# Optimization experiments

Hardware: AMD Instinct MI355X
Metric: run time of the kernel (lower is better)

The kernel has to match this reference:

```python
import jax, jax.numpy as jnp
import numpy as np

B, NW = 1024, 300
N = NW // 3          # 100 tokens (keypoints)
E = 5                # token dim after cat of PE(2): 3 + 2
H, D, L = 4, 64, 3   # heads, d_attention, layers


def setup_inputs() -> dict:
    key = jax.random.key(0)
    ks = jax.random.split(key, 8)
    s = jnp.float32(0.1)
    x = jax.random.normal(ks[0], (B, NW), dtype=jnp.float32)
    Wq = jax.random.normal(ks[1], (L, H, D, E), dtype=jnp.float32) * s  # per-head W_Q (no bias)
    Wk = jax.random.normal(ks[2], (L, H, D, E), dtype=jnp.float32) * s
    Wv = jax.random.normal(ks[3], (L, H, D, E), dtype=jnp.float32) * s
    Wo = jax.random.normal(ks[4], (L, E, H * D), dtype=jnp.float32) * s  # MHA output proj (no bias)
    Wf = jax.random.normal(ks[5], (L, E, E), dtype=jnp.float32) * s      # FFN linear
    bf = jax.random.normal(ks[6], (L, E), dtype=jnp.float32) * s
    g1 = jnp.ones((L, E), dtype=jnp.float32)
    b1 = jnp.zeros((L, E), dtype=jnp.float32)
    g2 = jnp.ones((L, E), dtype=jnp.float32)
    b2 = jnp.zeros((L, E), dtype=jnp.float32)
    return dict(x=x, Wq=Wq, Wk=Wk, Wv=Wv, Wo=Wo, Wf=Wf, bf=bf,
                g1=g1, b1=b1, g2=g2, b2=b2)


def _layer_norm(x, g, b, eps=1e-5):
    mu = jnp.mean(x, axis=-1, keepdims=True)
    var = jnp.mean((x - mu) ** 2, axis=-1, keepdims=True)  # biased, like torch LN
    return (x - mu) / jnp.sqrt(var + eps) * g + b


def reference(x, Wq, Wk, Wv, Wo, Wf, bf, g1, b1, g2, b2):
    kp = x.reshape(B, N, 3)                      # 'b (n d) -> b n d', d=3
    mask = kp[:, :, -1] > 0                      # [B,N] keypoint confidence mask
    # PositionalEncoding(d_model=2, kind='cat'): div_term=[1] -> pe=[sin(pos),cos(pos)]
    pos = jnp.arange(N, dtype=jnp.float32)
    pe = jnp.stack([jnp.sin(pos), jnp.cos(pos)], axis=-1)         # [N,2]
    out = jnp.concatenate([kp, jnp.broadcast_to(pe, (B, N, 2))], axis=-1)  # [B,N,5]
    out = jnp.where(mask[:, :, None], out, jnp.float32(0.0))      # out[~mask]=0

    pair = mask[:, None, None, :] & mask[:, None, :, None]        # [B,1,N,N]
    neg = -jnp.finfo(jnp.float32).max
    scale = jnp.float32(1.0 / np.sqrt(D))
    for l in range(L):
        # per-head projections (heads vectorized over h)
        q = jnp.einsum('bne,hde->bhnd', out, Wq[l])
        k = jnp.einsum('bne,hde->bhnd', out, Wk[l])
        v = jnp.einsum('bne,hde->bhnd', out, Wv[l])
        dots = jnp.einsum('bhid,bhjd->bhij', q, k) * scale        # [B,H,N,N]
        dots = jnp.where(pair, dots, neg)
        attn = jax.nn.softmax(dots, axis=-1)
        o = jnp.einsum('bhij,bhjd->bhid', attn, v)                # [B,H,N,D]
        o = o.transpose(0, 2, 1, 3).reshape(B, N, H * D)          # concat heads
        attn_out = o @ Wo[l].T                                    # [B,N,E]
        ln1 = _layer_norm(attn_out + out, g1[l], b1[l])
        ffn = jax.nn.relu(ln1 @ Wf[l].T + bf[l])
        out = _layer_norm(ffn + ln1, g2[l], b2[l])
    return out
```

## Files before the change

### kernel.cpp

```cpp
#include <hip/hip_runtime.h>
#include <math.h>

#define NTOK 100
#define EDIM 5
#define NH   4
#define NL   3
#define DD   64
#define BLK  256

__global__ void precompute_mp(const float* __restrict__ Wq,
                              const float* __restrict__ Wk,
                              const float* __restrict__ Wv,
                              const float* __restrict__ Wo,
                              float* __restrict__ mp) {
  const int blk = blockIdx.x;
  const int which = blk / 12;
  const int rem = blk % 12;
  const int l = rem / 4, h = rem % 4;
  const int t = threadIdx.x;

  __shared__ float A[320];
  __shared__ float Bsh[320];

  const float* wa = (which ? Wv : Wq) + (l*NH + h)*DD*EDIM;
  for (int r = t; r < 320; r += 64) A[r] = wa[r];
  if (which == 0) {
    const float* wk = Wk + (l*NH + h)*DD*EDIM;
    for (int r = t; r < 320; r += 64) Bsh[r] = wk[r];
  } else {
    for (int r = t; r < 320; r += 64) {
      int f = r >> 6, d = r & 63;
      Bsh[r] = Wo[(l*EDIM + f)*(NH*DD) + h*DD + d];
    }
  }
  __syncthreads();
  if (t < 25) {
    int e = t / 5, f = t % 5;
    float acc = 0.f;
    if (which == 0) {
      #pragma unroll 8
      for (int d = 0; d < DD; ++d) acc += A[d*5+e] * Bsh[d*5+f];
      acc *= 0.125f;
    } else {
      #pragma unroll 8
      for (int d = 0; d < DD; ++d) acc += A[d*5+e] * Bsh[f*64+d];
    }
    mp[which*960 + ((l*NH + h)*EDIM + e)*8 + f] = acc;
  }
}

__global__ __launch_bounds__(BLK) void encoder_kernel(
    const float* __restrict__ x,
    const float* __restrict__ mp,
    const float* __restrict__ Wf,
    const float* __restrict__ bfv,
    const float* __restrict__ g1,
    const float* __restrict__ b1,
    const float* __restrict__ g2,
    const float* __restrict__ b2,
    float* __restrict__ out)
{
  const int b = blockIdx.x, t = threadIdx.x;

  __shared__ float4 s_MP4[480];
  __shared__ float4 s_o4[NTOK+2];
  __shared__ float  s_o1[NTOK+2];
  __shared__ float4 s_w4[2][NH][NTOK+2];
  __shared__ float2 s_w2[2][NH][NTOK+2];
  __shared__ int    s_cidx[NTOK];
  __shared__ unsigned long long s_bal[2];

  const float* mpf = (const float*)s_MP4;

  for (int r = t; r < 480; r += BLK) s_MP4[r] = ((const float4*)mp)[r];

  float k0=0.f, k1=0.f, k2=0.f, msk=0.f;
  if (t < NTOK) {
    k0 = x[b*300 + 3*t];
    k1 = x[b*300 + 3*t + 1];
    k2 = x[b*300 + 3*t + 2];
    msk = (k2 > 0.f) ? 1.f : 0.f;
  }
  unsigned long long bal = __ballot(t < NTOK && msk != 0.f);
  if (t == 0)  s_bal[0] = bal;
  if (t == 64) s_bal[1] = bal;
  __syncthreads();
  const unsigned long long bw0 = s_bal[0], bw1 = s_bal[1];
  const int nm = __popcll(bw0) + __popcll(bw1);
  if (t < NTOK) {
    int lane = t & 63;
    unsigned long long lm = (lane == 0) ? 0ull : ((1ull << lane) - 1ull);
    int pre = (t < 64) ? __popcll(bw0 & lm) : (__popcll(bw0) + __popcll(bw1 & lm));
    if (msk != 0.f) {
      s_o4[pre] = make_float4(k0, k1, k2, sinf((float)t));
      s_o1[pre] = cosf((float)t);
      s_cidx[t] = pre;
    } else {
      s_cidx[t] = nm;
    }
  }
  if (t == 0) {
    s_o4[nm]   = make_float4(0.f,0.f,0.f,0.f); s_o1[nm]   = 0.f;
    s_o4[nm+1] = make_float4(0.f,0.f,0.f,0.f); s_o1[nm+1] = 0.f;
  }
  __syncthreads();

  const int hp   = (nm + 2) >> 1;
  const int natt = NH * hp;
  const int nsplit = (2*natt <= BLK) ? 2 : 1;
  const bool task = (t < natt*nsplit);
  int h = 0, i0 = 0, i1 = 0, i1r = 0, jlo = 0, jhi = 0;
  bool rep0 = false, rep1 = false, w1ok = false;
  if (task) {
    int g  = t / natt;
    int tt = t - g*natt;
    h = tt / hp; i0 = tt - h*hp; i1 = i0 + hp;
    i1r = (i1 <= nm) ? i1 : nm;
    w1ok = (i1 <= nm);
    rep0 = (i0 == nm); rep1 = (i1 == nm);
    int jmid = nm >> 1;
    if (nsplit == 2) { jlo = g ? jmid : 0; jhi = g ? nm : jmid; }
    else             { jlo = 0; jhi = nm; }
  }
  const int wg = task ? (t / natt) : 0;

  for (int l = 0; l < NL; ++l) {
    if (task) {
      const float* Mh = mpf + ((l*NH + h)*EDIM)*8;
      float4 oA = s_o4[i0];  float oA4 = s_o1[i0];
      float4 oB = s_o4[i1r]; float oB4 = s_o1[i1r];
      float oa[5] = {oA.x, oA.y, oA.z, oA.w, oA4};
      float ob[5] = {oB.x, oB.y, oB.z, oB.w, oB4};
      float a0[5], a1[5];
      #pragma unroll
      for (int f = 0; f < 5; ++f) { a0[f] = 0.f; a1[f] = 0.f; }
      #pragma unroll
      for (int e = 0; e < 5; ++e) {
        float4 mr = *(const float4*)(Mh + e*8); float m4 = Mh[e*8+4];
        float va = oa[e], vb = ob[e];
        a0[0] += va*mr.x; a0[1] += va*mr.y; a0[2] += va*mr.z; a0[3] += va*mr.w; a0[4] += va*m4;
        a1[0] += vb*mr.x; a1[1] += vb*mr.y; a1[2] += vb*mr.z; a1[3] += vb*mr.w; a1[4] += vb*m4;
      }

      float ls0=0.f, ls1=0.f;
      float w00=0.f,w01=0.f,w02=0.f,w03=0.f,w04=0.f;
      float w10=0.f,w11=0.f,w12=0.f,w13=0.f,w14=0.f;
      #pragma unroll 4
      for (int j = jlo; j < jhi; ++j) {
        float4 oj = s_o4[j]; float oe = s_o1[j];
        float s0 = a0[0]*oj.x + a0[1]*oj.y + a0[2]*oj.z + a0[3]*oj.w + a0[4]*oe;
        float s1 = a1[0]*oj.x + a1[1]*oj.y + a1[2]*oj.z + a1[3]*oj.w + a1[4]*oe;
        float p0 = rep0 ? 1.f : __expf(s0);
        float p1 = rep1 ? 1.f : __expf(s1);
        ls0 += p0; ls1 += p1;
        w00 += p0*oj.x; w01 += p0*oj.y; w02 += p0*oj.z; w03 += p0*oj.w; w04 += p0*oe;
        w10 += p1*oj.x; w11 += p1*oj.y; w12 += p1*oj.z; w13 += p1*oj.w; w14 += p1*oe;
      }
      s_w4[wg][h][i0] = make_float4(w00, w01, w02, w03);
      s_w2[wg][h][i0] = make_float2(w04, ls0);
      if (w1ok) {
        s_w4[wg][h][i1] = make_float4(w10, w11, w12, w13);
        s_w2[wg][h][i1] = make_float2(w14, ls1);
      }
    }
    __syncthreads();

    if (t <= nm) {
      int i = t;
      bool rep = (i == nm);
      float4 ov = s_o4[i]; float ov4 = s_o1[i];
      float o[5] = {ov.x, ov.y, ov.z, ov.w, ov4};
      float wext = rep ? (float)(NTOK - nm) : 0.f;
      float c[5] = {0.f, 0.f, 0.f, 0.f, 0.f};
      #pragma unroll
      for (int hh = 0; hh < NH; ++hh) {
        float4 wa = s_w4[0][hh][i]; float2 wb = s_w2[0][hh][i];
        float w[5] = {wa.x, wa.y, wa.z, wa.w, wb.x};
        float ls = wb.y;
        if (nsplit == 2) {
          float4 wa2 = s_w4[1][hh][i]; float2 wb2 = s_w2[1][hh][i];
          w[0] += wa2.x; w[1] += wa2.y; w[2] += wa2.z; w[3] += wa2.w; w[4] += wb2.x;
          ls += wb2.y;
        }
        #pragma unroll
        for (int e = 0; e < 5; ++e) w[e] += wext * o[e];
        float inv = 1.f / (rep ? (float)NTOK : ls);
        const float* Ph = mpf + 960 + ((l*NH + hh)*EDIM)*8;
        #pragma unroll
        for (int e = 0; e < 5; ++e) {
          float4 pr = *(const float4*)(Ph + e*8); float p4 = Ph[e*8+4];
          float we = w[e] * inv;
          c[0] += we*pr.x; c[1] += we*pr.y; c[2] += we*pr.z; c[3] += we*pr.w; c[4] += we*p4;
        }
      }
      float y[5];
      #pragma unroll
      for (int e = 0; e < 5; ++e) y[e] = o[e] + c[e];
      float mu = 0.2f*(y[0]+y[1]+y[2]+y[3]+y[4]);
      float var = 0.f;
      #pragma unroll
      for (int e = 0; e < 5; ++e) { float d = y[e]-mu; var += d*d; }
      var *= 0.2f;
      float inv = 1.f / sqrtf(var + 1e-5f);
      float ln1[5];
      #pragma unroll
      for (int e = 0; e < 5; ++e) ln1[e] = (y[e]-mu)*inv*g1[l*5+e] + b1[l*5+e];
      float r2[5];
      #pragma unroll
      for (int e = 0; e < 5; ++e) {
        float acc = bfv[l*5+e];
        #pragma unroll
        for (int f = 0; f < 5; ++f) acc += ln1[f]*Wf[(l*5+e)*5+f];
        acc = acc > 0.f ? acc : 0.f;
        r2[e] = acc + ln1[e];
      }
      float mu2 = 0.2f*(r2[0]+r2[1]+r2[2]+r2[3]+r2[4]);
      float var2 = 0.f;
      #pragma unroll
      for (int e = 0; e < 5; ++e) { float d = r2[e]-mu2; var2 += d*d; }
      var2 *= 0.2f;
      float inv2 = 1.f / sqrtf(var2 + 1e-5f);
      float no0 = (r2[0]-mu2)*inv2*g2[l*5+0] + b2[l*5+0];
      float no1 = (r2[1]-mu2)*inv2*g2[l*5+1] + b2[l*5+1];
      float no2 = (r2[2]-mu2)*inv2*g2[l*5+2] + b2[l*5+2];
      float no3 = (r2[3]-mu2)*inv2*g2[l*5+3] + b2[l*5+3];
      float no4 = (r2[4]-mu2)*inv2*g2[l*5+4] + b2[l*5+4];
      s_o4[i] = make_float4(no0, no1, no2, no3);
      s_o1[i] = no4;
    }
    __syncthreads();
  }

  for (int r = t; r < NTOK*EDIM; r += BLK) {
    int i = r / EDIM;
    int e = r - i*EDIM;
    int c = s_cidx[i];
    float v = (e < 4) ? ((const float*)&s_o4[c])[e] : s_o1[c];
    out[b*(NTOK*EDIM) + r] = v;
  }
}

extern "C" void kernel_launch(void* const* d_in, const int* in_sizes, int n_in,
                              void* d_out, int out_size, void* d_ws, size_t ws_size,
                              hipStream_t stream) {
  const float* x  = (const float*)d_in[0];
  const float* Wq = (const float*)d_in[1];
  const float* Wk = (const float*)d_in[2];
  const float* Wv = (const float*)d_in[3];
  const float* Wo = (const float*)d_in[4];
  const float* Wf = (const float*)d_in[5];
  const float* bf = (const float*)d_in[6];
  const float* g1 = (const float*)d_in[7];
  const float* b1 = (const float*)d_in[8];
  const float* g2 = (const float*)d_in[9];
  const float* b2 = (const float*)d_in[10];
  float* outp = (float*)d_out;
  float* mp   = (float*)d_ws;

  precompute_mp<<<24, 64, 0, stream>>>(Wq, Wk, Wv, Wo, mp);
  encoder_kernel<<<1024, BLK, 0, stream>>>(x, mp, Wf, bf, g1, b1, g2, b2, outp);
}
```

Measured before the change: 119.2 us.

## Map one wavefront per batch element and drop block barriers

The encoder kernel now processes four batch elements per block, one per 64-lane wavefront. Each lane owns a masked token and loops over all keys for all four heads, with a second token-per-lane path when more than 63 tokens survive the mask. This removes the per-layer __syncthreads and the cross-thread partial-sum exchange through shared memory. Attention scores are pre-scaled by log2(e) so the kernel can call the hardware exp2 directly. The cost is a quarter as many waves, leaving less latency hiding, and more serial work per lane.

```diff
diff --git a/kernel.cpp b/kernel.cpp
--- a/kernel.cpp
+++ b/kernel.cpp
@@ -7,6 +7,7 @@
 #define NL   3
 #define DD   64
 #define BLK  256
+#define LOG2E 1.4426950408889634f
 
 __global__ void precompute_mp(const float* __restrict__ Wq,
                               const float* __restrict__ Wk,
@@ -49,7 +50,7 @@
   }
 }
 
-__global__ __launch_bounds__(BLK) void encoder_kernel(
+__global__ __launch_bounds__(BLK, 1) void encoder_kernel(
     const float* __restrict__ x,
     const float* __restrict__ mp,
     const float* __restrict__ Wf,
@@ -60,183 +61,216 @@
     const float* __restrict__ b2,
     float* __restrict__ out)
 {
-  const int b = blockIdx.x, t = threadIdx.x;
-
-  __shared__ float4 s_MP4[480];
-  __shared__ float4 s_o4[NTOK+2];
-  __shared__ float  s_o1[NTOK+2];
-  __shared__ float4 s_w4[2][NH][NTOK+2];
-  __shared__ float2 s_w2[2][NH][NTOK+2];
-  __shared__ int    s_cidx[NTOK];
-  __shared__ unsigned long long s_bal[2];
-
-  const float* mpf = (const float*)s_MP4;
-
-  for (int r = t; r < 480; r += BLK) s_MP4[r] = ((const float4*)mp)[r];
-
-  float k0=0.f, k1=0.f, k2=0.f, msk=0.f;
-  if (t < NTOK) {
-    k0 = x[b*300 + 3*t];
-    k1 = x[b*300 + 3*t + 1];
-    k2 = x[b*300 + 3*t + 2];
-    msk = (k2 > 0.f) ? 1.f : 0.f;
-  }
-  unsigned long long bal = __ballot(t < NTOK && msk != 0.f);
-  if (t == 0)  s_bal[0] = bal;
-  if (t == 64) s_bal[1] = bal;
+  const int wv   = threadIdx.x >> 6;
+  const int lane = threadIdx.x & 63;
+  const int b    = blockIdx.x * 4 + wv;
+
+  __shared__ float s_mp[1920];
+  __shared__ float s_st[4][NTOK+1][8];
+  __shared__ int   s_cidx[4][NTOK];
+
+  for (int r = threadIdx.x; r < 480; r += BLK)
+    ((float4*)s_mp)[r] = ((const float4*)mp)[r];
   __syncthreads();
-  const unsigned long long bw0 = s_bal[0], bw1 = s_bal[1];
-  const int nm = __popcll(bw0) + __popcll(bw1);
-  if (t < NTOK) {
-    int lane = t & 63;
-    unsigned long long lm = (lane == 0) ? 0ull : ((1ull << lane) - 1ull);
-    int pre = (t < 64) ? __popcll(bw0 & lm) : (__popcll(bw0) + __popcll(bw1 & lm));
-    if (msk != 0.f) {
-      s_o4[pre] = make_float4(k0, k1, k2, sinf((float)t));
-      s_o1[pre] = cosf((float)t);
-      s_cidx[t] = pre;
+
+  float* st  = &s_st[wv][0][0];
+  int* cidx  = s_cidx[wv];
+
+  const float* xb = x + b*300;
+  const int t1 = lane, t2 = lane + 64;
+  float k0a = xb[3*t1], k1a = xb[3*t1+1], k2a = xb[3*t1+2];
+  bool m1 = (k2a > 0.f);
+  float k0b = 0.f, k1b = 0.f, k2b = 0.f; bool m2 = false;
+  if (t2 < NTOK) {
+    k0b = xb[3*t2]; k1b = xb[3*t2+1]; k2b = xb[3*t2+2];
+    m2 = (k2b > 0.f);
+  }
+  unsigned long long bm1 = __ballot(m1);
+  unsigned long long bm2 = __ballot(m2);
+  const int pc1 = __popcll(bm1);
+  const int nm  = pc1 + __popcll(bm2);
+  const int ns  = nm + 1;
+  unsigned long long below = (lane == 0) ? 0ull : ((1ull << lane) - 1ull);
+  int p1 = __popcll(bm1 & below);
+  int p2 = pc1 + __popcll(bm2 & below);
+  if (m1) {
+    *(float4*)(st + p1*8) = make_float4(k0a, k1a, k2a, sinf((float)t1));
+    st[p1*8+4] = cosf((float)t1);
+  }
+  cidx[t1] = m1 ? p1 : nm;
+  if (t2 < NTOK) {
+    if (m2) {
+      *(float4*)(st + p2*8) = make_float4(k0b, k1b, k2b, sinf((float)t2));
+      st[p2*8+4] = cosf((float)t2);
+    }
+    cidx[t2] = m2 ? p2 : nm;
+  }
+  if (lane == 0) {
+    *(float4*)(st + nm*8) = make_float4(0.f,0.f,0.f,0.f);
+    st[nm*8+4] = 0.f;
+  }
+
+  const bool slow = (ns > 64);
+  const int  rB   = lane + 64;
+  const bool act1 = (lane < ns);
+  const bool act2 = slow && (rB < ns);
+  const bool rep1 = (lane == nm);
+  const bool rep2 = (rB == nm);
+
+  float o[5], o2[5] = {0,0,0,0,0};
+  {
+    float4 v = *(const float4*)(st + lane*8);
+    o[0]=v.x; o[1]=v.y; o[2]=v.z; o[3]=v.w; o[4]=st[lane*8+4];
+  }
+  if (act2) {
+    float4 v = *(const float4*)(st + rB*8);
+    o2[0]=v.x; o2[1]=v.y; o2[2]=v.z; o2[3]=v.w; o2[4]=st[rB*8+4];
+  }
+
+  for (int l = 0; l < NL; ++l) {
+    float a[NH][5], a2[NH][5], w[NH][5], w2[NH][5], ls[NH], ls2[NH];
+    const float* Ml = s_mp + l*NH*40;
+
+    #pragma unroll
+    for (int h = 0; h < NH; ++h) {
+      const float* Mh = Ml + h*40;
+      float A0=0.f,A1=0.f,A2=0.f,A3=0.f,A4=0.f;
+      #pragma unroll
+      for (int e = 0; e < 5; ++e) {
+        float4 mr = *(const float4*)(Mh + e*8);
+        float  m4 = Mh[e*8+4];
+        A0 += o[e]*mr.x; A1 += o[e]*mr.y; A2 += o[e]*mr.z; A3 += o[e]*mr.w; A4 += o[e]*m4;
+      }
+      a[h][0]=A0*LOG2E; a[h][1]=A1*LOG2E; a[h][2]=A2*LOG2E;
+      a[h][3]=A3*LOG2E; a[h][4]=A4*LOG2E;
+      ls[h] = 0.f;
+      #pragma unroll
+      for (int f = 0; f < 5; ++f) w[h][f] = 0.f;
+    }
+    if (slow) {
+      #pragma unroll
+      for (int h = 0; h < NH; ++h) {
+        const float* Mh = Ml + h*40;
+        float A0=0.f,A1=0.f,A2=0.f,A3=0.f,A4=0.f;
+        #pragma unroll
+        for (int e = 0; e < 5; ++e) {
+          float4 mr = *(const float4*)(Mh + e*8);
+          float  m4 = Mh[e*8+4];
+          A0 += o2[e]*mr.x; A1 += o2[e]*mr.y; A2 += o2[e]*mr.z; A3 += o2[e]*mr.w; A4 += o2[e]*m4;
+        }
+        a2[h][0]=A0*LOG2E; a2[h][1]=A1*LOG2E; a2[h][2]=A2*LOG2E;
+        a2[h][3]=A3*LOG2E; a2[h][4]=A4*LOG2E;
+        ls2[h] = 0.f;
+        #pragma unroll
+        for (int f = 0; f < 5; ++f) w2[h][f] = 0.f;
+      }
+    }
+
+    if (!slow) {
+      #pragma unroll 2
+      for (int j = 0; j < nm; ++j) {
+        float4 oj4 = *(const float4*)(st + j*8);
+        float  oj5 = st[j*8+4];
+        float oj[5] = {oj4.x, oj4.y, oj4.z, oj4.w, oj5};
+        #pragma unroll
+        for (int h = 0; h < NH; ++h) {
+          float s = a[h][0]*oj[0]+a[h][1]*oj[1]+a[h][2]*oj[2]+a[h][3]*oj[3]+a[h][4]*oj[4];
+          float p = __builtin_amdgcn_exp2f(s);
+          p = rep1 ? 1.f : p;
+          ls[h] += p;
+          #pragma unroll
+          for (int e = 0; e < 5; ++e) w[h][e] += p*oj[e];
+        }
+      }
     } else {
-      s_cidx[t] = nm;
-    }
-  }
-  if (t == 0) {
-    s_o4[nm]   = make_float4(0.f,0.f,0.f,0.f); s_o1[nm]   = 0.f;
-    s_o4[nm+1] = make_float4(0.f,0.f,0.f,0.f); s_o1[nm+1] = 0.f;
-  }
-  __syncthreads();
-
-  const int hp   = (nm + 2) >> 1;
-  const int natt = NH * hp;
-  const int nsplit = (2*natt <= BLK) ? 2 : 1;
-  const bool task = (t < natt*nsplit);
-  int h = 0, i0 = 0, i1 = 0, i1r = 0, jlo = 0, jhi = 0;
-  bool rep0 = false, rep1 = false, w1ok = false;
-  if (task) {
-    int g  = t / natt;
-    int tt = t - g*natt;
-    h = tt / hp; i0 = tt - h*hp; i1 = i0 + hp;
-    i1r = (i1 <= nm) ? i1 : nm;
-    w1ok = (i1 <= nm);
-    rep0 = (i0 == nm); rep1 = (i1 == nm);
-    int jmid = nm >> 1;
-    if (nsplit == 2) { jlo = g ? jmid : 0; jhi = g ? nm : jmid; }
-    else             { jlo = 0; jhi = nm; }
-  }
-  const int wg = task ? (t / natt) : 0;
-
-  for (int l = 0; l < NL; ++l) {
-    if (task) {
-      const float* Mh = mpf + ((l*NH + h)*EDIM)*8;
-      float4 oA = s_o4[i0];  float oA4 = s_o1[i0];
-      float4 oB = s_o4[i1r]; float oB4 = s_o1[i1r];
-      float oa[5] = {oA.x, oA.y, oA.z, oA.w, oA4};
-      float ob[5] = {oB.x, oB.y, oB.z, oB.w, oB4};
-      float a0[5], a1[5];
-      #pragma unroll
-      for (int f = 0; f < 5; ++f) { a0[f] = 0.f; a1[f] = 0.f; }
-      #pragma unroll
-      for (int e = 0; e < 5; ++e) {
-        float4 mr = *(const float4*)(Mh + e*8); float m4 = Mh[e*8+4];
-        float va = oa[e], vb = ob[e];
-        a0[0] += va*mr.x; a0[1] += va*mr.y; a0[2] += va*mr.z; a0[3] += va*mr.w; a0[4] += va*m4;
-        a1[0] += vb*mr.x; a1[1] += vb*mr.y; a1[2] += vb*mr.z; a1[3] += vb*mr.w; a1[4] += vb*m4;
-      }
-
-      float ls0=0.f, ls1=0.f;
-      float w00=0.f,w01=0.f,w02=0.f,w03=0.f,w04=0.f;
-      float w10=0.f,w11=0.f,w12=0.f,w13=0.f,w14=0.f;
-      #pragma unroll 4
-      for (int j = jlo; j < jhi; ++j) {
-        float4 oj = s_o4[j]; float oe = s_o1[j];
-        float s0 = a0[0]*oj.x + a0[1]*oj.y + a0[2]*oj.z + a0[3]*oj.w + a0[4]*oe;
-        float s1 = a1[0]*oj.x + a1[1]*oj.y + a1[2]*oj.z + a1[3]*oj.w + a1[4]*oe;
-        float p0 = rep0 ? 1.f : __expf(s0);
-        float p1 = rep1 ? 1.f : __expf(s1);
-        ls0 += p0; ls1 += p1;
-        w00 += p0*oj.x; w01 += p0*oj.y; w02 += p0*oj.z; w03 += p0*oj.w; w04 += p0*oe;
-        w10 += p1*oj.x; w11 += p1*oj.y; w12 += p1*oj.z; w13 += p1*oj.w; w14 += p1*oe;
-      }
-      s_w4[wg][h][i0] = make_float4(w00, w01, w02, w03);
-      s_w2[wg][h][i0] = make_float2(w04, ls0);
-      if (w1ok) {
-        s_w4[wg][h][i1] = make_float4(w10, w11, w12, w13);
-        s_w2[wg][h][i1] = make_float2(w14, ls1);
-      }
-    }
-    __syncthreads();
-
-    if (t <= nm) {
-      int i = t;
-      bool rep = (i == nm);
-      float4 ov = s_o4[i]; float ov4 = s_o1[i];
-      float o[5] = {ov.x, ov.y, ov.z, ov.w, ov4};
-      float wext = rep ? (float)(NTOK - nm) : 0.f;
-      float c[5] = {0.f, 0.f, 0.f, 0.f, 0.f};
-      #pragma unroll
-      for (int hh = 0; hh < NH; ++hh) {
-        float4 wa = s_w4[0][hh][i]; float2 wb = s_w2[0][hh][i];
-        float w[5] = {wa.x, wa.y, wa.z, wa.w, wb.x};
-        float ls = wb.y;
-        if (nsplit == 2) {
-          float4 wa2 = s_w4[1][hh][i]; float2 wb2 = s_w2[1][hh][i];
-          w[0] += wa2.x; w[1] += wa2.y; w[2] += wa2.z; w[3] += wa2.w; w[4] += wb2.x;
-          ls += wb2.y;
-        }
-        #pragma unroll
-        for (int e = 0; e < 5; ++e) w[e] += wext * o[e];
-        float inv = 1.f / (rep ? (float)NTOK : ls);
-        const float* Ph = mpf + 960 + ((l*NH + hh)*EDIM)*8;
-        #pragma unroll
-        for (int e = 0; e < 5; ++e) {
-          float4 pr = *(const float4*)(Ph + e*8); float p4 = Ph[e*8+4];
-          float we = w[e] * inv;
-          c[0] += we*pr.x; c[1] += we*pr.y; c[2] += we*pr.z; c[3] += we*pr.w; c[4] += we*p4;
+      #pragma unroll 2
+      for (int j = 0; j < nm; ++j) {
+        float4 oj4 = *(const float4*)(st + j*8);
+        float  oj5 = st[j*8+4];
+        float oj[5] = {oj4.x, oj4.y, oj4.z, oj4.w, oj5};
+        #pragma unroll
+        for (int h = 0; h < NH; ++h) {
+          float sA = a[h][0]*oj[0]+a[h][1]*oj[1]+a[h][2]*oj[2]+a[h][3]*oj[3]+a[h][4]*oj[4];
+          float sB = a2[h][0]*oj[0]+a2[h][1]*oj[1]+a2[h][2]*oj[2]+a2[h][3]*oj[3]+a2[h][4]*oj[4];
+          float pA = __builtin_amdgcn_exp2f(sA);
+          float pB = __builtin_amdgcn_exp2f(sB);
+          pB = rep2 ? 1.f : pB;
+          ls[h] += pA; ls2[h] += pB;
+          #pragma unroll
+          for (int e = 0; e < 5; ++e) { w[h][e] += pA*oj[e]; w2[h][e] += pB*oj[e]; }
+        }
+      }
+    }
+
+    auto token_pass = [&](float* o_, float (*w_)[5], float* ls_,
+                          bool isrep, bool active, int row) {
+      float wext = isrep ? (float)(NTOK - nm) : 0.f;
+      float c[5] = {0.f,0.f,0.f,0.f,0.f};
+      const float* Pl = s_mp + 960 + l*NH*40;
+      #pragma unroll
+      for (int h = 0; h < NH; ++h) {
+        float inv = isrep ? 0.01f : 1.f/ls_[h];
+        const float* Ph = Pl + h*40;
+        #pragma unroll
+        for (int f = 0; f < 5; ++f) {
+          float wn = (w_[h][f] + wext*o_[f]) * inv;
+          float4 pr = *(const float4*)(Ph + f*8);
+          float  p4 = Ph[f*8+4];
+          c[0]+=wn*pr.x; c[1]+=wn*pr.y; c[2]+=wn*pr.z; c[3]+=wn*pr.w; c[4]+=wn*p4;
         }
       }
       float y[5];
       #pragma unroll
-      for (int e = 0; e < 5; ++e) y[e] = o[e] + c[e];
+      for (int e = 0; e < 5; ++e) y[e] = o_[e] + c[e];
       float mu = 0.2f*(y[0]+y[1]+y[2]+y[3]+y[4]);
       float var = 0.f;
       #pragma unroll
       for (int e = 0; e < 5; ++e) { float d = y[e]-mu; var += d*d; }
       var *= 0.2f;
-      float inv = 1.f / sqrtf(var + 1e-5f);
+      float inv1 = 1.f/sqrtf(var + 1e-5f);
       float ln1[5];
       #pragma unroll
-      for (int e = 0; e < 5; ++e) ln1[e] = (y[e]-mu)*inv*g1[l*5+e] + b1[l*5+e];
-      float r2[5];
+      for (int e = 0; e < 5; ++e) ln1[e] = (y[e]-mu)*inv1*g1[l*5+e] + b1[l*5+e];
+      float rr[5];
       #pragma unroll
       for (int e = 0; e < 5; ++e) {
         float acc = bfv[l*5+e];
         #pragma unroll
         for (int f = 0; f < 5; ++f) acc += ln1[f]*Wf[(l*5+e)*5+f];
         acc = acc > 0.f ? acc : 0.f;
-        r2[e] = acc + ln1[e];
-      }
-      float mu2 = 0.2f*(r2[0]+r2[1]+r2[2]+r2[3]+r2[4]);
+        rr[e] = acc + ln1[e];
+      }
+      float mu2 = 0.2f*(rr[0]+rr[1]+rr[2]+rr[3]+rr[4]);
       float var2 = 0.f;
       #pragma unroll
-      for (int e = 0; e < 5; ++e) { float d = r2[e]-mu2; var2 += d*d; }
+      for (int e = 0; e < 5; ++e) { float d = rr[e]-mu2; var2 += d*d; }
       var2 *= 0.2f;
-      float inv2 = 1.f / sqrtf(var2 + 1e-5f);
-      float no0 = (r2[0]-mu2)*inv2*g2[l*5+0] + b2[l*5+0];
-      float no1 = (r2[1]-mu2)*inv2*g2[l*5+1] + b2[l*5+1];
-      float no2 = (r2[2]-mu2)*inv2*g2[l*5+2] + b2[l*5+2];
-      float no3 = (r2[3]-mu2)*inv2*g2[l*5+3] + b2[l*5+3];
-      float no4 = (r2[4]-mu2)*inv2*g2[l*5+4] + b2[l*5+4];
-      s_o4[i] = make_float4(no0, no1, no2, no3);
-      s_o1[i] = no4;
-    }
-    __syncthreads();
-  }
-
-  for (int r = t; r < NTOK*EDIM; r += BLK) {
-    int i = r / EDIM;
-    int e = r - i*EDIM;
-    int c = s_cidx[i];
-    float v = (e < 4) ? ((const float*)&s_o4[c])[e] : s_o1[c];
-    out[b*(NTOK*EDIM) + r] = v;
+      float inv2 = 1.f/sqrtf(var2 + 1e-5f);
+      float n0 = (rr[0]-mu2)*inv2*g2[l*5+0] + b2[l*5+0];
+      float n1 = (rr[1]-mu2)*inv2*g2[l*5+1] + b2[l*5+1];
+      float n2 = (rr[2]-mu2)*inv2*g2[l*5+2] + b2[l*5+2];
+      float n3 = (rr[3]-mu2)*inv2*g2[l*5+3] + b2[l*5+3];
+      float n4 = (rr[4]-mu2)*inv2*g2[l*5+4] + b2[l*5+4];
+      o_[0]=n0; o_[1]=n1; o_[2]=n2; o_[3]=n3; o_[4]=n4;
+      if (active) {
+        *(float4*)(st + row*8) = make_float4(n0,n1,n2,n3);
+        st[row*8+4] = n4;
+      }
+    };
+    token_pass(o,  w,  ls,  rep1, act1, lane);
+    if (slow) token_pass(o2, w2, ls2, rep2, act2, rB);
+  }
+
+  const int obase = b*(NTOK*EDIM);
+  #pragma unroll
+  for (int rr = 0; rr < 8; ++rr) {
+    int idx = rr*64 + lane;
+    if (idx < NTOK*EDIM) {
+      int tok = idx / 5;
+      int e = idx - tok*5;
+      int c = cidx[tok];
+      out[obase + idx] = st[c*8 + e];
+    }
   }
 }
 
@@ -258,5 +292,5 @@
   float* mp   = (float*)d_ws;
 
   precompute_mp<<<24, 64, 0, stream>>>(Wq, Wk, Wv, Wo, mp);
-  encoder_kernel<<<1024, BLK, 0, stream>>>(x, mp, Wf, bf, g1, b1, g2, b2, outp);
+  encoder_kernel<<<256, BLK, 0, stream>>>(x, mp, Wf, bf, g1, b1, g2, b2, outp);
 }
```

New measurement: 132.4 us. +11.1%, slower.
